# Performance work log

Hardware: AMD Instinct MI355X
Metric: run time of the kernel (lower is better)

## Reference

```python
import jax, jax.numpy as jnp
import numpy as np

# Model / simulation constants (globals in the original repo)
B = 64
N_INPUTS = 784
N_HIDDEN = 2048
N_OUTPUTS = 10
N_NEURONS = N_HIDDEN + N_OUTPUTS
E = 262144          # number of recurrent edges
T_MAX = 30          # simulation steps
VMAX = 1.0
THRESH = 0.25
TAU = 5.0
DT = 0.5            # dt*vmax = 0.5 matches the 0.5-spaced delay grid


def setup_inputs() -> dict:
    key = jax.random.key(0)
    k = jax.random.split(key, 7)
    x = jax.random.normal(k[0], (B, N_INPUTS), jnp.float32)
    # recurrent edge list: sources are hidden neurons only (output rows zeroed in A),
    # targets may be any hidden or output neuron
    src = jax.random.randint(k[1], (E,), 0, N_HIDDEN)
    tgt = jax.random.randint(k[2], (E,), 0, N_NEURONS)
    # axonal delays drawn from arange(3.0, 8.0, 0.5) as in initialise_edges
    delays = jnp.arange(3.0, 8.0, 0.5, dtype=jnp.float32)
    L_e = delays[jax.random.randint(k[3], (E,), 0, delays.shape[0])]
    # signed uniform weights: uniform(0,1) * (+1/-1)
    sign = jnp.where(jax.random.uniform(k[4], (E,)) > 0.5, 1.0, -1.0).astype(jnp.float32)
    W_e = jax.random.uniform(k[5], (E,), dtype=jnp.float32) * sign
    input_W = (jax.random.uniform(k[6], (N_INPUTS, N_HIDDEN), dtype=jnp.float32,
                                  minval=-1.0, maxval=1.0) * 0.1)
    return {"x": x, "input_W": input_W, "W_e": W_e, "L_e": L_e,
            "src": src, "tgt": tgt}


def _snn_forward(x, input_W, W_e, L_e, src, tgt):
    # (B, n_hidden) input current, injected every 3rd step (phase == 2)
    input_currents = x @ input_W

    def step(carry, _):
        S, V, Vm, acc, phase = carry
        # edges whose traveling spike has reached its delay
        arrived = jnp.isclose(S, L_e, atol=1e-5, rtol=1e-8)          # (B, E) bool
        spikes = V * arrived * W_e                                   # (B, E)
        I_syn = jnp.zeros((B, N_NEURONS), spikes.dtype).at[:, tgt].add(spikes)
        I_syn = I_syn.at[:, :N_HIDDEN].add(jnp.where(phase == 2, input_currents, 0.0))
        # leaky integration
        Vm = Vm + (-Vm + I_syn) * (DT / TAU)
        V_exc = jnp.maximum(0.0, Vm - THRESH)
        fired = (V_exc > 0).at[:, -N_OUTPUTS:].set(False)            # outputs never spike
        # eval mode: dropout_rate == 0 -> no_dropout branch of lax.cond
        idle = S == 0
        newS = fired[:, src] & idle                                  # launch spike on idle edges
        S = S * ~arrived
        V = V * ~arrived
        acc = acc + Vm[:, -N_OUTPUTS:]
        Vm = Vm - Vm * fired - 0.2 * fired                           # reset + afterhyperpolarization
        S = S + (S > 0) * DT * VMAX + newS * DT * VMAX               # advance traveling spikes
        V = V + newS * V_exc[:, src]
        return (S, V, Vm, acc, (phase + 1) % 3), None

    carry0 = (jnp.zeros((B, E), jnp.float32),
              jnp.zeros((B, E), jnp.float32),
              jnp.zeros((B, N_NEURONS), jnp.float32),
              jnp.zeros((B, N_OUTPUTS), jnp.float32),
              jnp.asarray(0, jnp.int32))
    step_ck = jax.checkpoint(step, prevent_cse=False)
    (_, _, _, acc, _), _ = jax.lax.scan(step_ck, carry0, None, length=T_MAX)
    return acc / T_MAX


def reference(x, input_W, W_e, L_e, src, tgt):
    return _snn_forward(x, input_W, W_e, L_e, src, tgt)
```

## Files before the change

kernel.cpp:

```cpp
#include <hip/hip_runtime.h>
#include <hip/hip_cooperative_groups.h>

namespace cg = cooperative_groups;

static constexpr int B_    = 64;
static constexpr int NIN   = 784;
static constexpr int NH    = 2048;
static constexpr int NOUT  = 10;
static constexpr int NN    = 2058;
static constexpr int NE    = 262144;
static constexpr int CAP   = 208;
static constexpr int SB    = 64;
static constexpr int NRAIL = NH * 10;

static constexpr int PARTS = 2;
static constexpr int OWN   = NH / PARTS;
static constexpr int STPB  = 1024;
static constexpr int GRID  = B_ * PARTS;

static constexpr size_t IC_OFF    = 0;
static constexpr size_t ERECT_OFF = IC_OFF + (size_t)B_ * NH;
static constexpr size_t CUR_OFF   = ERECT_OFF + 2ull * CAP * NN;
static constexpr size_t BAR_OFF   = CUR_OFF + NN + 8;
static constexpr size_t TABG_OFF  = (BAR_OFF + 64 * 16 + 63) & ~(size_t)63;

__device__ __forceinline__ float ld_agent(const float* p) {
    return __hip_atomic_load(p, __ATOMIC_RELAXED, __HIP_MEMORY_SCOPE_AGENT);
}
__device__ __forceinline__ void st_agent(float* p, float v) {
    __hip_atomic_store(p, v, __ATOMIC_RELAXED, __HIP_MEMORY_SCOPE_AGENT);
}

__device__ __forceinline__ void demux8(const float tv[8], const float w8[8],
                                       float Ia[6]) {
    #pragma unroll
    for (int u = 0; u < 8; ++u) {
        const unsigned uw = __float_as_uint(tv[u]);
        const int tau = uw & 7;
        const float vw = __uint_as_float(uw & ~7u) * w8[u];
        #pragma unroll
        for (int jt = 0; jt < 6; ++jt)
            Ia[jt] += (tau == jt) ? vw : 0.f;
    }
}

__device__ __forceinline__ void lds8(const float* __restrict__ tab,
                                     const int4 q[4], float tv[8], float w8[8]) {
    #pragma unroll
    for (int u = 0; u < 4; ++u) {
        tv[2 * u]     = *(const float*)((const char*)tab + q[u].x);
        tv[2 * u + 1] = *(const float*)((const char*)tab + q[u].z);
        w8[2 * u]     = __int_as_float(q[u].y);
        w8[2 * u + 1] = __int_as_float(q[u].w);
    }
}

__device__ __forceinline__ void gather_col(const int4* __restrict__ pcol,
                                           const float* __restrict__ tab,
                                           int deg, float Ia[6]) {
    const int it = (deg + 7) >> 3;
    if (it <= 0) return;
    const int4* p = pcol;
    int4 qc[4], qn[4];
    float tvp[8], wp[8], tvc[8], wc[8];
    #pragma unroll
    for (int u = 0; u < 4; ++u) qc[u] = p[(size_t)u * NN];
    lds8(tab, qc, tvp, wp);
    if (it > 1) {
        p += (size_t)4 * NN;
        #pragma unroll
        for (int u = 0; u < 4; ++u) qc[u] = p[(size_t)u * NN];
    }
    for (int i = 1; i < it; ++i) {
        if (i + 1 < it) {
            const int4* pn = p + (size_t)4 * NN;
            #pragma unroll
            for (int u = 0; u < 4; ++u) qn[u] = pn[(size_t)u * NN];
        }
        lds8(tab, qc, tvc, wc);
        demux8(tvp, wp, Ia);
        #pragma unroll
        for (int u = 0; u < 8; ++u) { tvp[u] = tvc[u]; wp[u] = wc[u]; }
        #pragma unroll
        for (int u = 0; u < 4; ++u) qc[u] = qn[u];
        p += (size_t)4 * NN;
    }
    demux8(tvp, wp, Ia);
}

__global__ __launch_bounds__(STPB, 4) void fused_kernel(
    const float* __restrict__ x, const float* __restrict__ inW,
    const int* __restrict__ src, const int* __restrict__ tgt,
    const float* __restrict__ We, const float* __restrict__ Le,
    float* __restrict__ IC, int* __restrict__ cnt,
    int2* __restrict__ erec2, int* __restrict__ bar,
    float* __restrict__ tabG, float* __restrict__ out)
{
    cg::grid_group grid = cg::this_grid();
    const int bid = blockIdx.x;
    const int tid = threadIdx.x;
    __shared__ float tab[NRAIL];

    {
        float4* z = (float4*)erec2;
        const int n4 = (int)((2ull * CAP * NN + NN + 8 + 64 * 16 + 3) / 4);
        const int stride = GRID * STPB;
        for (int i = bid * STPB + tid; i < n4; i += stride)
            z[i] = float4{0.f, 0.f, 0.f, 0.f};
    }
    grid.sync();

    if (bid < SB) {
        int* lh    = (int*)tab;
        int* lbase = lh + NN;
        for (int i = tid; i < NN; i += STPB) lh[i] = 0;
        __syncthreads();
        const int base = bid * (NE / SB);
        for (int k = 0; k < NE / SB; k += STPB)
            atomicAdd(&lh[tgt[base + k + tid]], 1);
        __syncthreads();
        for (int i = tid; i < NN; i += STPB) {
            const int c = lh[i];
            lbase[i] = c ? atomicAdd(&cnt[i], c) : 0;
            lh[i] = 0;
        }
        __syncthreads();
        for (int k = 0; k < NE / SB; k += STPB) {
            const int e  = base + k + tid;
            const int tg = tgt[e];
            const int p  = lbase[tg] + atomicAdd(&lh[tg], 1);
            const int d  = (int)(Le[e] * 2.0f + 0.5f);
            if (p < CAP)
                erec2[((size_t)(p >> 1) * NN + tg) * 2 + (p & 1)] =
                    make_int2((src[e] + (d - 6) * NH) * 4,
                              __float_as_int(We[e]));
        }
    } else {
        const int gb = bid - SB;
        const int nc = gb & 7;
        const int bb = (gb >> 3) * 8;
        const int sl = tid >> 8;
        const int t  = tid & 255;
        const int n  = nc * 256 + t;
        const int b0 = bb + sl * 2;
        float a0 = 0.f, a1 = 0.f;
        #pragma unroll 16
        for (int kk = 0; kk < NIN; ++kk) {
            const float w = inW[(size_t)kk * NH + n];
            a0 = fmaf(x[b0 * NIN + kk],       w, a0);
            a1 = fmaf(x[(b0 + 1) * NIN + kk], w, a1);
        }
        IC[(size_t)b0 * NH + n]       = a0;
        IC[(size_t)(b0 + 1) * NH + n] = a1;
    }
    grid.sync();

    const int b    = bid >> 1;
    const int part = bid & 1;
    const int lane = tid & 63;
    const int wv   = tid >> 6;

    const int4* __restrict__ erec4 = (const int4*)erec2;
    const int n    = part * OWN + tid;
    const float ic = IC[(size_t)b * NH + n];
    const int deg  = min(cnt[n], CAP);

    const int o = wv;
    const bool oWave = (part == 0) && (wv < NOUT);
    const int degO = oWave ? min(cnt[NH + o], CAP) : 0;

    int pa[10]; float pv[10];
    #pragma unroll
    for (int j = 0; j < 10; ++j) { pa[j] = -1; pv[j] = 0.f; }
    float Vm = 0.f, Vo = 0.f, acc = 0.f;

    int* const barb = bar + b * 16;
    const int peerBase = (part ^ 1) * OWN;

    for (int k = 0; k < 5; ++k) {
        const int t0 = 6 * k;
        float Ia[6] = {}, Io[6] = {};

        if (k) {
            if (tid == 0)
                while (__hip_atomic_load(barb, __ATOMIC_RELAXED,
                                         __HIP_MEMORY_SCOPE_AGENT) < 2 * k)
                    __builtin_amdgcn_s_sleep(1);
            __syncthreads();

            const float* gr = tabG + ((size_t)((k - 1) & 1) * B_ + b) * 10 * NH;
            const int nn = peerBase + tid;
            #pragma unroll
            for (int j = 0; j < 10; ++j)
                tab[j * NH + nn] = ld_agent(gr + (size_t)j * NH + nn);
            __syncthreads();

            gather_col(erec4 + n, tab, deg, Ia);
            if (oWave) {
                const int2* __restrict__ e2 = (const int2*)erec4;
                for (int i = lane; i < degO; i += 64) {
                    const int2 r = e2[((size_t)(i >> 1) * NN + NH + o) * 2 + (i & 1)];
                    const unsigned uw =
                        __float_as_uint(*(const float*)((const char*)tab + r.x));
                    const int tau = uw & 7;
                    const float vw = __uint_as_float(uw & ~7u) * __int_as_float(r.y);
                    #pragma unroll
                    for (int jt = 0; jt < 6; ++jt)
                        Io[jt] += (tau == jt) ? vw : 0.f;
                }
                #pragma unroll
                for (int jt = 0; jt < 6; ++jt) {
                    #pragma unroll
                    for (int off = 32; off > 0; off >>= 1)
                        Io[jt] += __shfl_xor(Io[jt], off, 64);
                }
            }
        }

        #pragma unroll
        for (int j = 0; j < 6; ++j) {
            const int t = t0 + j;
            const bool inj = (j == 2 || j == 5);
            const float I = Ia[j] + (inj ? ic : 0.f);
            Vm += (I - Vm) * 0.1f;
            const float vx = fmaxf(Vm - 0.25f, 0.f);
            const bool f = vx > 0.f;
            #pragma unroll
            for (int jd = 0; jd < 10; ++jd)
                if (f & (t > pa[jd])) { pa[jd] = t + jd + 6; pv[jd] = vx; }
            if (f) Vm = -0.2f;
            if (oWave) { Vo += (Io[j] - Vo) * 0.1f; acc += Vo; }
        }

        if (k < 4) {
            __syncthreads();
            const int t0n = t0 + 6;
            float* gw = tabG + ((size_t)(k & 1) * B_ + b) * 10 * NH;
            #pragma unroll
            for (int j = 0; j < 10; ++j) {
                const unsigned u1 = (unsigned)(pa[j] - t0n);
                const unsigned c1 = (u1 < 6u) ? u1 : 7u;
                const float packed =
                    __uint_as_float((__float_as_uint(pv[j]) & ~7u) | c1);
                tab[j * NH + n] = packed;
                st_agent(gw + (size_t)j * NH + n, packed);
            }
            asm volatile("s_waitcnt vmcnt(0)" ::: "memory");
            __syncthreads();
            if (tid == 0)
                __hip_atomic_fetch_add(barb, 1, __ATOMIC_RELAXED,
                                       __HIP_MEMORY_SCOPE_AGENT);
        }
    }

    if (oWave && lane == 0) out[b * NOUT + o] = acc * (1.0f / 30.0f);
}

extern "C" void kernel_launch(void* const* d_in, const int* in_sizes, int n_in,
                              void* d_out, int out_size, void* d_ws, size_t ws_size,
                              hipStream_t stream) {
    const float* x   = (const float*)d_in[0];
    const float* inW = (const float*)d_in[1];
    const float* We  = (const float*)d_in[2];
    const float* Le  = (const float*)d_in[3];
    const int*   src = (const int*)d_in[4];
    const int*   tgt = (const int*)d_in[5];

    float* ws    = (float*)d_ws;
    float* IC    = ws + IC_OFF;
    int2*  erec2 = (int2*)(ws + ERECT_OFF);
    int*   cnt   = (int*)(ws + CUR_OFF);
    int*   bar   = (int*)(ws + BAR_OFF);
    float* tabG  = ws + TABG_OFF;
    float* out   = (float*)d_out;

    void* kargs[] = { (void*)&x, (void*)&inW, (void*)&src, (void*)&tgt,
                      (void*)&We, (void*)&Le, (void*)&IC, (void*)&cnt,
                      (void*)&erec2, (void*)&bar, (void*)&tabG, (void*)&out };
    hipLaunchCooperativeKernel((const void*)fused_kernel,
                               dim3(GRID), dim3(STPB), kargs, 0, stream);
}
```

Before: 314.7 us.

## Split each batch across four blocks with two threads per neuron gather

Grows the grid from 2 to 4 blocks per batch row, so each block owns 512 hidden neurons. Each neuron's edge gather is split between two threads, and the halves are combined through shared memory. Every block now reloads the full spike table from global memory each chunk, and the input projection is spread over more blocks with one batch row per thread. The aim is more parallelism in the latency-bound gather, at the cost of more inter-block barrier traffic and larger global table reads.

```diff
diff --git a/kernel.cpp b/kernel.cpp
--- a/kernel.cpp
+++ b/kernel.cpp
@@ -10,11 +10,11 @@
 static constexpr int NN    = 2058;
 static constexpr int NE    = 262144;
 static constexpr int CAP   = 208;
-static constexpr int SB    = 64;
+static constexpr int SB    = 128;
 static constexpr int NRAIL = NH * 10;
 
-static constexpr int PARTS = 2;
-static constexpr int OWN   = NH / PARTS;
+static constexpr int PARTS = 4;
+static constexpr int OWN   = 512;
 static constexpr int STPB  = 1024;
 static constexpr int GRID  = B_ * PARTS;
 
@@ -100,6 +100,7 @@
     const int bid = blockIdx.x;
     const int tid = threadIdx.x;
     __shared__ float tab[NRAIL];
+    __shared__ float cmb[6 * OWN];
 
     {
         float4* z = (float4*)erec2;
@@ -138,36 +139,36 @@
     } else {
         const int gb = bid - SB;
         const int nc = gb & 7;
-        const int bb = (gb >> 3) * 8;
+        const int bc = gb >> 3;
         const int sl = tid >> 8;
         const int t  = tid & 255;
         const int n  = nc * 256 + t;
-        const int b0 = bb + sl * 2;
-        float a0 = 0.f, a1 = 0.f;
+        const int b0 = bc * 4 + sl;
+        float a0 = 0.f;
         #pragma unroll 16
-        for (int kk = 0; kk < NIN; ++kk) {
-            const float w = inW[(size_t)kk * NH + n];
-            a0 = fmaf(x[b0 * NIN + kk],       w, a0);
-            a1 = fmaf(x[(b0 + 1) * NIN + kk], w, a1);
-        }
-        IC[(size_t)b0 * NH + n]       = a0;
-        IC[(size_t)(b0 + 1) * NH + n] = a1;
+        for (int kk = 0; kk < NIN; ++kk)
+            a0 = fmaf(x[b0 * NIN + kk], inW[(size_t)kk * NH + n], a0);
+        IC[(size_t)b0 * NH + n] = a0;
     }
     grid.sync();
 
-    const int b    = bid >> 1;
-    const int part = bid & 1;
+    const int b    = bid >> 2;
+    const int part = bid & 3;
     const int lane = tid & 63;
     const int wv   = tid >> 6;
+    const bool owner = tid < OWN;
+    const int nl   = tid & (OWN - 1);
 
     const int4* __restrict__ erec4 = (const int4*)erec2;
-    const int n    = part * OWN + tid;
-    const float ic = IC[(size_t)b * NH + n];
+    const int n    = part * OWN + nl;
     const int deg  = min(cnt[n], CAP);
-
-    const int o = wv;
-    const bool oWave = (part == 0) && (wv < NOUT);
-    const int degO = oWave ? min(cnt[NH + o], CAP) : 0;
+    const int it   = (deg + 7) >> 3;
+    const int hlow = (it + 1) >> 1;
+    const float ic = owner ? IC[(size_t)b * NH + n] : 0.f;
+
+    const bool oW = (part == 0 && wv < 8) || (part == 1 && wv < 2);
+    const int o = (part == 0) ? wv : 8 + wv;
+    const int degO = oW ? min(cnt[NH + o], CAP) : 0;
 
     int pa[10]; float pv[10];
     #pragma unroll
@@ -175,7 +176,6 @@
     float Vm = 0.f, Vo = 0.f, acc = 0.f;
 
     int* const barb = bar + b * 16;
-    const int peerBase = (part ^ 1) * OWN;
 
     for (int k = 0; k < 5; ++k) {
         const int t0 = 6 * k;
@@ -184,19 +184,26 @@
         if (k) {
             if (tid == 0)
                 while (__hip_atomic_load(barb, __ATOMIC_RELAXED,
-                                         __HIP_MEMORY_SCOPE_AGENT) < 2 * k)
+                                         __HIP_MEMORY_SCOPE_AGENT) < 4 * k)
                     __builtin_amdgcn_s_sleep(1);
             __syncthreads();
 
             const float* gr = tabG + ((size_t)((k - 1) & 1) * B_ + b) * 10 * NH;
-            const int nn = peerBase + tid;
             #pragma unroll
-            for (int j = 0; j < 10; ++j)
-                tab[j * NH + nn] = ld_agent(gr + (size_t)j * NH + nn);
-            __syncthreads();
-
-            gather_col(erec4 + n, tab, deg, Ia);
-            if (oWave) {
+            for (int j = 0; j < 10; ++j) {
+                tab[j * NH + tid]        = ld_agent(gr + (size_t)j * NH + tid);
+                tab[j * NH + 1024 + tid] = ld_agent(gr + (size_t)j * NH + 1024 + tid);
+            }
+            __syncthreads();
+
+            if (owner) {
+                gather_col(erec4 + n, tab, min(deg, 8 * hlow), Ia);
+            } else {
+                const int dh = deg - 8 * hlow;
+                if (dh > 0)
+                    gather_col(erec4 + n + (size_t)4 * NN * hlow, tab, dh, Ia);
+            }
+            if (oW) {
                 const int2* __restrict__ e2 = (const int2*)erec4;
                 for (int i = lane; i < degO; i += 64) {
                     const int2 r = e2[((size_t)(i >> 1) * NN + NH + o) * 2 + (i & 1)];
@@ -215,35 +222,45 @@
                         Io[jt] += __shfl_xor(Io[jt], off, 64);
                 }
             }
-        }
-
-        #pragma unroll
-        for (int j = 0; j < 6; ++j) {
-            const int t = t0 + j;
-            const bool inj = (j == 2 || j == 5);
-            const float I = Ia[j] + (inj ? ic : 0.f);
-            Vm += (I - Vm) * 0.1f;
-            const float vx = fmaxf(Vm - 0.25f, 0.f);
-            const bool f = vx > 0.f;
+            if (!owner) {
+                #pragma unroll
+                for (int jt = 0; jt < 6; ++jt) cmb[jt * OWN + nl] = Ia[jt];
+            }
+            __syncthreads();
+            if (owner) {
+                #pragma unroll
+                for (int jt = 0; jt < 6; ++jt) Ia[jt] += cmb[jt * OWN + nl];
+            }
+        }
+
+        if (owner) {
             #pragma unroll
-            for (int jd = 0; jd < 10; ++jd)
-                if (f & (t > pa[jd])) { pa[jd] = t + jd + 6; pv[jd] = vx; }
-            if (f) Vm = -0.2f;
-            if (oWave) { Vo += (Io[j] - Vo) * 0.1f; acc += Vo; }
+            for (int j = 0; j < 6; ++j) {
+                const int t = t0 + j;
+                const bool inj = (j == 2 || j == 5);
+                const float I = Ia[j] + (inj ? ic : 0.f);
+                Vm += (I - Vm) * 0.1f;
+                const float vx = fmaxf(Vm - 0.25f, 0.f);
+                const bool f = vx > 0.f;
+                #pragma unroll
+                for (int jd = 0; jd < 10; ++jd)
+                    if (f & (t > pa[jd])) { pa[jd] = t + jd + 6; pv[jd] = vx; }
+                if (f) Vm = -0.2f;
+                if (oW) { Vo += (Io[j] - Vo) * 0.1f; acc += Vo; }
+            }
         }
 
         if (k < 4) {
-            __syncthreads();
             const int t0n = t0 + 6;
             float* gw = tabG + ((size_t)(k & 1) * B_ + b) * 10 * NH;
-            #pragma unroll
-            for (int j = 0; j < 10; ++j) {
-                const unsigned u1 = (unsigned)(pa[j] - t0n);
-                const unsigned c1 = (u1 < 6u) ? u1 : 7u;
-                const float packed =
-                    __uint_as_float((__float_as_uint(pv[j]) & ~7u) | c1);
-                tab[j * NH + n] = packed;
-                st_agent(gw + (size_t)j * NH + n, packed);
+            if (owner) {
+                #pragma unroll
+                for (int j = 0; j < 10; ++j) {
+                    const unsigned u1 = (unsigned)(pa[j] - t0n);
+                    const unsigned c1 = (u1 < 6u) ? u1 : 7u;
+                    st_agent(gw + (size_t)j * NH + n,
+                             __uint_as_float((__float_as_uint(pv[j]) & ~7u) | c1));
+                }
             }
             asm volatile("s_waitcnt vmcnt(0)" ::: "memory");
             __syncthreads();
@@ -253,7 +270,7 @@
         }
     }
 
-    if (oWave && lane == 0) out[b * NOUT + o] = acc * (1.0f / 30.0f);
+    if (oW && lane == 0) out[b * NOUT + o] = acc * (1.0f / 30.0f);
 }
 
 extern "C" void kernel_launch(void* const* d_in, const int* in_sizes, int n_in,
```

New measurement: 279.1 us. 11.3% less time.
